# Performance work log

Measured on AMD Instinct MI355X. Metric: run time of the kernel, lower is better.

The kernel has to match this reference:

```python
import jax, jax.numpy as jnp
import numpy as np

HEADS = 16
DIM = 1024
D_K = DIM // HEADS
SEQ = 2048


def setup_inputs() -> dict:
    key = jax.random.key(0)
    ks = jax.random.split(key, 11)
    s = 1.0 / np.sqrt(DIM).astype(np.float32)
    return {
        "q": jax.random.normal(ks[0], (SEQ, DIM), jnp.float32),
        "k": jax.random.normal(ks[1], (SEQ, DIM), jnp.float32),
        "v": jax.random.normal(ks[2], (SEQ, DIM), jnp.float32),
        "Wq": jax.random.normal(ks[3], (DIM, DIM), jnp.float32) * s,
        "bq": jax.random.normal(ks[4], (DIM,), jnp.float32) * 0.01,
        "Wk": jax.random.normal(ks[5], (DIM, DIM), jnp.float32) * s,
        "bk": jax.random.normal(ks[6], (DIM,), jnp.float32) * 0.01,
        "Wv": jax.random.normal(ks[7], (DIM, DIM), jnp.float32) * s,
        "bv": jax.random.normal(ks[8], (DIM,), jnp.float32) * 0.01,
        "Wo": jax.random.normal(ks[9], (DIM, DIM), jnp.float32) * s,
        "bo": jax.random.normal(ks[10], (DIM,), jnp.float32) * 0.01,
    }


def reference(q, k, v, Wq, bq, Wk, bk, Wv, bv, Wo, bo):
    S = q.shape[0]
    # torch Linear: x @ W.T + b; view to (1, S, H, d_k) then transpose to (1, H, S, d_k)
    def proj(x, W, b):
        return (x @ W.T + b).reshape(1, S, HEADS, D_K).transpose(0, 2, 1, 3)

    qh = proj(q, Wq, bq)  # (1, H, S, d)
    kh = proj(k, Wk, bk)
    vh = proj(v, Wv, bv)

    scale = 1.0 / np.sqrt(D_K).astype(np.float32)
    scores = jnp.einsum("bhqd,bhkd->bhqk", qh, kh) * scale  # (1, H, S, S)
    # NOTE: source applies softmax over dim=1 == the HEADS axis (faithful quirk)
    attn = jax.nn.softmax(scores, axis=1)
    ctx = jnp.einsum("bhqk,bhkd->bhqd", attn, vh)  # (1, H, S, d)
    concat = ctx.transpose(0, 2, 1, 3).reshape(1, S, DIM)
    return concat @ Wo.T + bo
```

## Files before the change

### kernel.cpp

```cpp
#include <hip/hip_runtime.h>
#include <hip/hip_fp16.h>


typedef _Float16 f16;
typedef _Float16 f16x4 __attribute__((ext_vector_type(4)));
typedef _Float16 f16x8 __attribute__((ext_vector_type(8)));
typedef float    f32x4 __attribute__((ext_vector_type(4)));

#define S_LEN 2048
#define DIM   1024
#define NH    16
#define DK    64
#define SCALE 0.125f

#define MFMA(a, b, c) __builtin_amdgcn_mfma_f32_16x16x32_f16(a, b, c, 0, 0, 0)

typedef __attribute__((address_space(1))) void g_void;
typedef __attribute__((address_space(3))) void l_void;

static __device__ __forceinline__ void gload_lds16(const void* g, void* l) {
  __builtin_amdgcn_global_load_lds((g_void*)g, (l_void*)l, 16, 0, 0);
}

__global__ __launch_bounds__(256) void cvt_all(
    const float* __restrict__ q, const float* __restrict__ k, const float* __restrict__ v,
    const float* __restrict__ Wq, const float* __restrict__ Wk, const float* __restrict__ Wv,
    const float* __restrict__ Wo, f16* __restrict__ qh, f16* __restrict__ kh,
    f16* __restrict__ vh, f16* __restrict__ wqh, f16* __restrict__ wkh,
    f16* __restrict__ wvh, f16* __restrict__ woh) {
  const size_t M = 1048576;
  const int seg = blockIdx.y;
  const float* src;
  f16* dst;
  switch (seg) {
    case 0: src = q;      dst = qh;      break;
    case 1: src = q + M;  dst = qh + M;  break;
    case 2: src = k;      dst = kh;      break;
    case 3: src = k + M;  dst = kh + M;  break;
    case 4: src = v;      dst = vh;      break;
    case 5: src = v + M;  dst = vh + M;  break;
    case 6: src = Wq;     dst = wqh;     break;
    case 7: src = Wk;     dst = wkh;     break;
    case 8: src = Wv;     dst = wvh;     break;
    default: src = Wo;    dst = woh;     break;
  }
  int i = blockIdx.x * 256 + threadIdx.x;
  float4 vv = ((const float4*)src)[i];
  f16x4 o = {(f16)vv.x, (f16)vv.y, (f16)vv.z, (f16)vv.w};
  ((f16x4*)dst)[i] = o;
}

__global__ __launch_bounds__(256) void cvt_f32_f16(const float* __restrict__ src,
                                                   f16* __restrict__ dst, int n4) {
  int i = blockIdx.x * 256 + threadIdx.x;
  if (i < n4) {
    float4 v = ((const float4*)src)[i];
    f16x4 o = {(f16)v.x, (f16)v.y, (f16)v.z, (f16)v.w};
    ((f16x4*)dst)[i] = o;
  }
}

static __device__ __forceinline__ void gemm64_core(const f16* __restrict__ X,
                                                   const f16* __restrict__ W,
                                                   int k0, int k1, int bm, int bn,
                                                   f16* As2, f16* Bs2,
                                                   f32x4 (&acc)[4][2]) {
  const int tid = threadIdx.x;
  const int wv = tid >> 6;
  const int lane = tid & 63;
  const int qd = lane >> 4;
  const int l16 = lane & 15;
  const int wm = (wv & 1) * 64;
  const int wn = (wv >> 1) * 32;
  const int lr4 = lane >> 2, lc4 = lane & 3;
  const int kkw = wv & 1;
  const int rgw = wv >> 1;

  const f16* gA = X + (size_t)(bm + rgw * 64 + lr4) * DIM + k0 + kkw * 32 + lc4 * 8;
  const f16* gB = W + (size_t)(bn + rgw * 32 + lr4) * DIM + k0 + kkw * 32 + lc4 * 8;
  f16* lA = As2 + kkw * (128 * 32) + (rgw * 64) * 32;
  f16* lB = Bs2 + kkw * (64 * 32) + (rgw * 32) * 32;

  for (int kt = k0; kt < k1; kt += 64) {
#pragma unroll
    for (int t = 0; t < 4; t++)
      gload_lds16(gA + t * 16 * DIM, lA + t * 16 * 32);
#pragma unroll
    for (int t = 0; t < 2; t++)
      gload_lds16(gB + t * 16 * DIM, lB + t * 16 * 32);
    gA += 64;
    gB += 64;
    __syncthreads();

    f16x8 af[4][2], bf[2][2];
#pragma unroll
    for (int mi = 0; mi < 4; mi++)
#pragma unroll
      for (int kk = 0; kk < 2; kk++)
        af[mi][kk] = *(const f16x8*)&As2[kk * (128 * 32) + (wm + mi * 16 + l16) * 32 + qd * 8];
#pragma unroll
    for (int ni = 0; ni < 2; ni++)
#pragma unroll
      for (int kk = 0; kk < 2; kk++)
        bf[ni][kk] = *(const f16x8*)&Bs2[kk * (64 * 32) + (wn + ni * 16 + l16) * 32 + qd * 8];
#pragma unroll
    for (int mi = 0; mi < 4; mi++)
#pragma unroll
      for (int ni = 0; ni < 2; ni++) {
        acc[mi][ni] = MFMA(af[mi][0], bf[ni][0], acc[mi][ni]);
        acc[mi][ni] = MFMA(af[mi][1], bf[ni][1], acc[mi][ni]);
      }
    __syncthreads();
  }
}

__global__ __launch_bounds__(256) void gemm_qkv(
    const f16* __restrict__ X0, const f16* __restrict__ X1, const f16* __restrict__ X2,
    const f16* __restrict__ W0, const f16* __restrict__ W1, const f16* __restrict__ W2,
    const float* __restrict__ b0, const float* __restrict__ b1, const float* __restrict__ b2,
    f16* __restrict__ o0, f16* __restrict__ o1, f16* __restrict__ o2) {
  __shared__ __align__(16) f16 As2[2 * 128 * 32];
  __shared__ __align__(16) f16 Bs2[2 * 64 * 32];
  const int z = blockIdx.z;
  const f16* X = z == 0 ? X0 : z == 1 ? X1 : X2;
  const f16* W = z == 0 ? W0 : z == 1 ? W1 : W2;
  const float* bias = z == 0 ? b0 : z == 1 ? b1 : b2;
  f16* outh = z == 0 ? o0 : z == 1 ? o1 : o2;

  const int bm = blockIdx.y * 128, bn = blockIdx.x * 64;
  f32x4 acc[4][2];
#pragma unroll
  for (int a = 0; a < 4; a++)
#pragma unroll
    for (int b = 0; b < 2; b++) acc[a][b] = (f32x4){0.f, 0.f, 0.f, 0.f};

  gemm64_core(X, W, 0, DIM, bm, bn, As2, Bs2, acc);

  const int tid = threadIdx.x;
  const int wv = tid >> 6, lane = tid & 63;
  const int qd = lane >> 4, l16 = lane & 15;
  const int wm = (wv & 1) * 64, wn = (wv >> 1) * 32;
#pragma unroll
  for (int mi = 0; mi < 4; mi++) {
#pragma unroll
    for (int ni = 0; ni < 2; ni++) {
      const int gm = bm + wm + mi * 16 + qd * 4;
      const int gn = bn + wn + ni * 16 + l16;
      const float bs = bias[gn];
      if (z == 2) {
        f16x4 o = {(f16)(acc[mi][ni][0] + bs), (f16)(acc[mi][ni][1] + bs),
                   (f16)(acc[mi][ni][2] + bs), (f16)(acc[mi][ni][3] + bs)};
        *(f16x4*)&outh[(size_t)gn * S_LEN + gm] = o;
      } else {
#pragma unroll
        for (int r = 0; r < 4; r++)
          outh[(size_t)(gm + r) * DIM + gn] = (f16)(acc[mi][ni][r] + bs);
      }
    }
  }
}

__global__ __launch_bounds__(256) void gemm_out(const f16* __restrict__ X,
                                                const f16* __restrict__ W,
                                                const float* __restrict__ bias,
                                                float* __restrict__ outf) {
  __shared__ __align__(16) f16 As2[2 * 128 * 32];
  __shared__ __align__(16) f16 Bs2[2 * 64 * 32];
  const int z = blockIdx.z;
  const int bm = blockIdx.y * 128, bn = blockIdx.x * 64;
  f32x4 acc[4][2];
#pragma unroll
  for (int a = 0; a < 4; a++)
#pragma unroll
    for (int b = 0; b < 2; b++) acc[a][b] = (f32x4){0.f, 0.f, 0.f, 0.f};

  gemm64_core(X, W, z * (DIM / 2), (z + 1) * (DIM / 2), bm, bn, As2, Bs2, acc);

  const int tid = threadIdx.x;
  const int wv = tid >> 6, lane = tid & 63;
  const int qd = lane >> 4, l16 = lane & 15;
  const int wm = (wv & 1) * 64, wn = (wv >> 1) * 32;
#pragma unroll
  for (int mi = 0; mi < 4; mi++) {
#pragma unroll
    for (int ni = 0; ni < 2; ni++) {
      const int gm = bm + wm + mi * 16 + qd * 4;
      const int gn = bn + wn + ni * 16 + l16;
      const float bs = z == 0 ? bias[gn] : 0.f;
#pragma unroll
      for (int r = 0; r < 4; r++)
        atomicAdd(&outf[(size_t)(gm + r) * DIM + gn], acc[mi][ni][r] + bs);
    }
  }
}

__global__ __launch_bounds__(256) void attn_denom(const f16* __restrict__ Qp,
                                                  const f16* __restrict__ Kp,
                                                  f16* __restrict__ IDn) {
  __shared__ __align__(16) f16 Qs[2][2][64 * 32];
  __shared__ __align__(16) f16 Ks[2][2][64 * 32];
  const int tid = threadIdx.x;
  const int wv = tid >> 6;
  const int lane = tid & 63;
  const int qd = lane >> 4;
  const int l16 = lane & 15;
  const int wm = (wv & 1) * 32, wn = (wv >> 1) * 32;
  const int bi = blockIdx.y * 64, bj = blockIdx.x * 64;
  const int lr4 = lane >> 2, lc4 = lane & 3;
  const int hhw = wv & 1;
  const int kkw = wv >> 1;

  f32x4 dsum[2][2];
#pragma unroll
  for (int a = 0; a < 2; a++)
#pragma unroll
    for (int b = 0; b < 2; b++) dsum[a][b] = (f32x4){0.f, 0.f, 0.f, 0.f};

  for (int h0 = 0; h0 < NH; h0 += 2) {
    const int hcol = (h0 + hhw) * DK + kkw * 32;
    const f16* gq = Qp + (size_t)(bi + lr4) * DIM + hcol + lc4 * 8;
    const f16* gk = Kp + (size_t)(bj + lr4) * DIM + hcol + lc4 * 8;
#pragma unroll
    for (int t = 0; t < 4; t++) {
      gload_lds16(gq + (size_t)t * 16 * DIM, &Qs[hhw][kkw][t * 16 * 32]);
      gload_lds16(gk + (size_t)t * 16 * DIM, &Ks[hhw][kkw][t * 16 * 32]);
    }
    __syncthreads();

#pragma unroll
    for (int hh = 0; hh < 2; hh++) {
      f16x8 af[2][2], bf[2][2];
#pragma unroll
      for (int mi = 0; mi < 2; mi++)
#pragma unroll
        for (int kk = 0; kk < 2; kk++)
          af[mi][kk] = *(const f16x8*)&Qs[hh][kk][(wm + mi * 16 + l16) * 32 + qd * 8];
#pragma unroll
      for (int ni = 0; ni < 2; ni++)
#pragma unroll
        for (int kk = 0; kk < 2; kk++)
          bf[ni][kk] = *(const f16x8*)&Ks[hh][kk][(wn + ni * 16 + l16) * 32 + qd * 8];
#pragma unroll
      for (int mi = 0; mi < 2; mi++)
#pragma unroll
        for (int ni = 0; ni < 2; ni++) {
          f32x4 s = {0.f, 0.f, 0.f, 0.f};
          s = MFMA(af[mi][0], bf[ni][0], s);
          s = MFMA(af[mi][1], bf[ni][1], s);
#pragma unroll
          for (int r = 0; r < 4; r++) dsum[mi][ni][r] += __expf(s[r] * SCALE);
        }
    }
    __syncthreads();
  }
#pragma unroll
  for (int mi = 0; mi < 2; mi++)
#pragma unroll
    for (int ni = 0; ni < 2; ni++)
#pragma unroll
      for (int r = 0; r < 4; r++) {
        const int gi = bi + wm + mi * 16 + qd * 4 + r;
        const int gj = bj + wn + ni * 16 + l16;
        IDn[(size_t)gi * S_LEN + gj] = (f16)(1.f / dsum[mi][ni][r]);
      }
}

__global__ __launch_bounds__(256) void attn_ctx(const f16* __restrict__ Qp,
                                                const f16* __restrict__ Kp,
                                                const f16* __restrict__ Vt,
                                                const f16* __restrict__ IDn,
                                                float* __restrict__ Cp) {
  __shared__ __align__(16) f16 Ks[2][64 * 32];
  __shared__ __align__(16) f16 Vs[2][64 * 32];
  __shared__ __align__(16) f16 Is[2][128 * 32];
  __shared__ __align__(16) f16 Pl[4][32 * 32];
  const int tid = threadIdx.x;
  const int wv = tid >> 6;
  const int lane = tid & 63;
  const int qd = lane >> 4;
  const int l16 = lane & 15;
  const int h = blockIdx.y;
  const int i0 = blockIdx.x * 128;
  const int iw = i0 + wv * 32;
  const int jb = blockIdx.z * 512;
  const int lr4 = lane >> 2, lc4 = lane & 3;
  const int sw = wv & 1;
  const int gw = wv >> 1;
  f16* pl = Pl[wv];

  f16x8 aq[2][2];
#pragma unroll
  for (int mi = 0; mi < 2; mi++)
#pragma unroll
    for (int kk = 0; kk < 2; kk++)
      aq[mi][kk] = *(const f16x8*)(Qp + (size_t)(iw + mi * 16 + l16) * DIM +
                                   h * DK + kk * 32 + qd * 8);

  f32x4 acc[2][4];
#pragma unroll
  for (int a = 0; a < 2; a++)
#pragma unroll
    for (int b = 0; b < 4; b++) acc[a][b] = (f32x4){0.f, 0.f, 0.f, 0.f};

  for (int jt = 0; jt < 8; jt++) {
    const int j0 = jb + jt * 64;
#pragma unroll
    for (int t = 0; t < 2; t++)
      gload_lds16(Kp + (size_t)(j0 + gw * 32 + t * 16 + lr4) * DIM + h * DK + sw * 32 + lc4 * 8,
                  &Ks[sw][(gw * 32 + t * 16) * 32]);
#pragma unroll
    for (int t = 0; t < 2; t++)
      gload_lds16(Vt + (size_t)(h * DK + gw * 32 + t * 16 + lr4) * S_LEN + j0 + sw * 32 + lc4 * 8,
                  &Vs[sw][(gw * 32 + t * 16) * 32]);
#pragma unroll
    for (int t = 0; t < 4; t++)
      gload_lds16(IDn + (size_t)(i0 + gw * 64 + t * 16 + lr4) * S_LEN + j0 + sw * 32 + lc4 * 8,
                  &Is[sw][(gw * 64 + t * 16) * 32]);
    __syncthreads();

#pragma unroll
    for (int sub = 0; sub < 2; sub++) {
      f16x8 bk[2][2];
#pragma unroll
      for (int ni = 0; ni < 2; ni++)
#pragma unroll
        for (int kk = 0; kk < 2; kk++)
          bk[ni][kk] = *(const f16x8*)&Ks[kk][(sub * 32 + ni * 16 + l16) * 32 + qd * 8];
#pragma unroll
      for (int mi = 0; mi < 2; mi++)
#pragma unroll
        for (int ni = 0; ni < 2; ni++) {
          f32x4 s = {0.f, 0.f, 0.f, 0.f};
          s = MFMA(aq[mi][0], bk[ni][0], s);
          s = MFMA(aq[mi][1], bk[ni][1], s);
#pragma unroll
          for (int r = 0; r < 4; r++)
            pl[(mi * 16 + qd * 4 + r) * 32 + ni * 16 + l16] = (f16)__expf(s[r] * SCALE);
        }

      f16x8 bv[4];
#pragma unroll
      for (int nd = 0; nd < 4; nd++)
        bv[nd] = *(const f16x8*)&Vs[sub][(nd * 16 + l16) * 32 + qd * 8];
#pragma unroll
      for (int mi = 0; mi < 2; mi++) {
        f16x8 ef = *(const f16x8*)&pl[(mi * 16 + l16) * 32 + qd * 8];
        f16x8 idn = *(const f16x8*)&Is[sub][(wv * 32 + mi * 16 + l16) * 32 + qd * 8];
        f16x8 p = ef * idn;
#pragma unroll
        for (int nd = 0; nd < 4; nd++)
          acc[mi][nd] = MFMA(p, bv[nd], acc[mi][nd]);
      }
    }
    __syncthreads();
  }

#pragma unroll
  for (int mi = 0; mi < 2; mi++)
#pragma unroll
    for (int nd = 0; nd < 4; nd++)
#pragma unroll
      for (int r = 0; r < 4; r++)
        atomicAdd(&Cp[(size_t)(iw + mi * 16 + qd * 4 + r) * DIM + h * DK + nd * 16 + l16],
                  acc[mi][nd][r]);
}

extern "C" void kernel_launch(void* const* d_in, const int* in_sizes, int n_in,
                              void* d_out, int out_size, void* d_ws, size_t ws_size,
                              hipStream_t stream) {
  const float* q  = (const float*)d_in[0];
  const float* k  = (const float*)d_in[1];
  const float* v  = (const float*)d_in[2];
  const float* Wq = (const float*)d_in[3];
  const float* bq = (const float*)d_in[4];
  const float* Wk = (const float*)d_in[5];
  const float* bk = (const float*)d_in[6];
  const float* Wv = (const float*)d_in[7];
  const float* bv = (const float*)d_in[8];
  const float* Wo = (const float*)d_in[9];
  const float* bo = (const float*)d_in[10];
  float* out = (float*)d_out;

  f16* w = (f16*)d_ws;
  f16* qh  = w;
  f16* kh  = qh + (size_t)S_LEN * DIM;
  f16* vh  = kh + (size_t)S_LEN * DIM;
  f16* wqh = vh + (size_t)S_LEN * DIM;
  f16* wkh = wqh + (size_t)DIM * DIM;
  f16* wvh = wkh + (size_t)DIM * DIM;
  f16* woh = wvh + (size_t)DIM * DIM;
  f16* Qp  = woh + (size_t)DIM * DIM;
  f16* Kp  = Qp + (size_t)S_LEN * DIM;
  f16* Vt  = Kp + (size_t)S_LEN * DIM;
  f16* IDn = qh;
  float* Cp = (float*)vh;
  f16* Ct  = qh;

  dim3 b256(256);
  cvt_all<<<dim3(1024, 10), b256, 0, stream>>>(q, k, v, Wq, Wk, Wv, Wo,
                                               qh, kh, vh, wqh, wkh, wvh, woh);

  gemm_qkv<<<dim3(DIM / 64, S_LEN / 128, 3), b256, 0, stream>>>(
      qh, kh, vh, wqh, wkh, wvh, bq, bk, bv, Qp, Kp, Vt);

  hipMemsetAsync(Cp, 0, (size_t)S_LEN * DIM * sizeof(float), stream);
  hipMemsetAsync(out, 0, (size_t)S_LEN * DIM * sizeof(float), stream);

  attn_denom<<<dim3(S_LEN / 64, S_LEN / 64), b256, 0, stream>>>(Qp, Kp, IDn);
  attn_ctx<<<dim3(S_LEN / 128, NH, 4), b256, 0, stream>>>(Qp, Kp, Vt, IDn, Cp);

  const int nqkv4 = S_LEN * DIM / 4;
  cvt_f32_f16<<<nqkv4 / 256, b256, 0, stream>>>(Cp, Ct, nqkv4);

  gemm_out<<<dim3(DIM / 64, S_LEN / 128, 2), b256, 0, stream>>>(Ct, woh, bo, out);
}
```

Measured before the change: 233.3 us.

## Double-buffer LDS loads in attention kernels and load inverse denominators directly

Result: slower. 258.4 us (+10.8%).

```diff
diff --git a/kernel.cpp b/kernel.cpp
--- a/kernel.cpp
+++ b/kernel.cpp
@@ -14,6 +14,9 @@
 #define SCALE 0.125f
 
 #define MFMA(a, b, c) __builtin_amdgcn_mfma_f32_16x16x32_f16(a, b, c, 0, 0, 0)
+
+#define VM_WAIT0   asm volatile("s_waitcnt vmcnt(0)" ::: "memory")
+#define WG_BARRIER asm volatile("s_barrier" ::: "memory")
 
 typedef __attribute__((address_space(1))) void g_void;
 typedef __attribute__((address_space(3))) void l_void;
@@ -207,8 +210,8 @@
   const int wm = (wv & 1) * 32, wn = (wv >> 1) * 32;
   const int bi = blockIdx.y * 64, bj = blockIdx.x * 64;
   const int lr4 = lane >> 2, lc4 = lane & 3;
-  const int hhw = wv & 1;
-  const int kkw = wv >> 1;
+  const int kkw = wv & 1;
+  const int q0 = (wv >> 1) * 2;
 
   f32x4 dsum[2][2];
 #pragma unroll
@@ -216,42 +219,53 @@
 #pragma unroll
     for (int b = 0; b < 2; b++) dsum[a][b] = (f32x4){0.f, 0.f, 0.f, 0.f};
 
-  for (int h0 = 0; h0 < NH; h0 += 2) {
-    const int hcol = (h0 + hhw) * DK + kkw * 32;
-    const f16* gq = Qp + (size_t)(bi + lr4) * DIM + hcol + lc4 * 8;
-    const f16* gk = Kp + (size_t)(bj + lr4) * DIM + hcol + lc4 * 8;
-#pragma unroll
-    for (int t = 0; t < 4; t++) {
-      gload_lds16(gq + (size_t)t * 16 * DIM, &Qs[hhw][kkw][t * 16 * 32]);
-      gload_lds16(gk + (size_t)t * 16 * DIM, &Ks[hhw][kkw][t * 16 * 32]);
-    }
-    __syncthreads();
-
-#pragma unroll
-    for (int hh = 0; hh < 2; hh++) {
-      f16x8 af[2][2], bf[2][2];
-#pragma unroll
-      for (int mi = 0; mi < 2; mi++)
-#pragma unroll
-        for (int kk = 0; kk < 2; kk++)
-          af[mi][kk] = *(const f16x8*)&Qs[hh][kk][(wm + mi * 16 + l16) * 32 + qd * 8];
-#pragma unroll
-      for (int ni = 0; ni < 2; ni++)
-#pragma unroll
-        for (int kk = 0; kk < 2; kk++)
-          bf[ni][kk] = *(const f16x8*)&Ks[hh][kk][(wn + ni * 16 + l16) * 32 + qd * 8];
-#pragma unroll
-      for (int mi = 0; mi < 2; mi++)
-#pragma unroll
-        for (int ni = 0; ni < 2; ni++) {
-          f32x4 s = {0.f, 0.f, 0.f, 0.f};
-          s = MFMA(af[mi][0], bf[ni][0], s);
-          s = MFMA(af[mi][1], bf[ni][1], s);
-#pragma unroll
-          for (int r = 0; r < 4; r++) dsum[mi][ni][r] += __expf(s[r] * SCALE);
-        }
-    }
-    __syncthreads();
+  {
+    const f16* gq = Qp + (size_t)(bi + q0 * 16 + lr4) * DIM + 0 * DK + kkw * 32 + lc4 * 8;
+    const f16* gk = Kp + (size_t)(bj + q0 * 16 + lr4) * DIM + 0 * DK + kkw * 32 + lc4 * 8;
+#pragma unroll
+    for (int t = 0; t < 2; t++) {
+      gload_lds16(gq + (size_t)t * 16 * DIM, &Qs[0][kkw][(q0 + t) * 16 * 32]);
+      gload_lds16(gk + (size_t)t * 16 * DIM, &Ks[0][kkw][(q0 + t) * 16 * 32]);
+    }
+  }
+
+#pragma unroll
+  for (int h = 0; h < NH; h++) {
+    const int buf = h & 1;
+    VM_WAIT0;
+    WG_BARRIER;
+
+    if (h + 1 < NH) {
+      const f16* gq = Qp + (size_t)(bi + q0 * 16 + lr4) * DIM + (h + 1) * DK + kkw * 32 + lc4 * 8;
+      const f16* gk = Kp + (size_t)(bj + q0 * 16 + lr4) * DIM + (h + 1) * DK + kkw * 32 + lc4 * 8;
+#pragma unroll
+      for (int t = 0; t < 2; t++) {
+        gload_lds16(gq + (size_t)t * 16 * DIM, &Qs[buf ^ 1][kkw][(q0 + t) * 16 * 32]);
+        gload_lds16(gk + (size_t)t * 16 * DIM, &Ks[buf ^ 1][kkw][(q0 + t) * 16 * 32]);
+      }
+    }
+
+    f16x8 af[2][2], bf[2][2];
+#pragma unroll
+    for (int mi = 0; mi < 2; mi++)
+#pragma unroll
+      for (int kk = 0; kk < 2; kk++)
+        af[mi][kk] = *(const f16x8*)&Qs[buf][kk][(wm + mi * 16 + l16) * 32 + qd * 8];
+#pragma unroll
+    for (int ni = 0; ni < 2; ni++)
+#pragma unroll
+      for (int kk = 0; kk < 2; kk++)
+        bf[ni][kk] = *(const f16x8*)&Ks[buf][kk][(wn + ni * 16 + l16) * 32 + qd * 8];
+#pragma unroll
+    for (int mi = 0; mi < 2; mi++)
+#pragma unroll
+      for (int ni = 0; ni < 2; ni++) {
+        f32x4 s = {0.f, 0.f, 0.f, 0.f};
+        s = MFMA(af[mi][0], bf[ni][0], s);
+        s = MFMA(af[mi][1], bf[ni][1], s);
+#pragma unroll
+        for (int r = 0; r < 4; r++) dsum[mi][ni][r] += __expf(s[r] * SCALE);
+      }
   }
 #pragma unroll
   for (int mi = 0; mi < 2; mi++)
@@ -265,15 +279,14 @@
       }
 }
 
-__global__ __launch_bounds__(256) void attn_ctx(const f16* __restrict__ Qp,
-                                                const f16* __restrict__ Kp,
-                                                const f16* __restrict__ Vt,
-                                                const f16* __restrict__ IDn,
-                                                float* __restrict__ Cp) {
-  __shared__ __align__(16) f16 Ks[2][64 * 32];
+__global__ __launch_bounds__(256, 4) void attn_ctx(const f16* __restrict__ Qp,
+                                                   const f16* __restrict__ Kp,
+                                                   const f16* __restrict__ Vt,
+                                                   const f16* __restrict__ IDn,
+                                                   float* __restrict__ Cp) {
+  __shared__ __align__(16) f16 Ks[2][2][32 * 32];
   __shared__ __align__(16) f16 Vs[2][64 * 32];
-  __shared__ __align__(16) f16 Is[2][128 * 32];
-  __shared__ __align__(16) f16 Pl[4][32 * 32];
+  __shared__ __align__(16) f16 Pl[4][32 * 40];
   const int tid = threadIdx.x;
   const int wv = tid >> 6;
   const int lane = tid & 63;
@@ -284,8 +297,8 @@
   const int iw = i0 + wv * 32;
   const int jb = blockIdx.z * 512;
   const int lr4 = lane >> 2, lc4 = lane & 3;
-  const int sw = wv & 1;
-  const int gw = wv >> 1;
+  const int kkw = wv & 1;
+  const int rhw = wv >> 1;
   f16* pl = Pl[wv];
 
   f16x8 aq[2][2];
@@ -302,57 +315,67 @@
 #pragma unroll
     for (int b = 0; b < 4; b++) acc[a][b] = (f32x4){0.f, 0.f, 0.f, 0.f};
 
-  for (int jt = 0; jt < 8; jt++) {
-    const int j0 = jb + jt * 64;
-#pragma unroll
-    for (int t = 0; t < 2; t++)
-      gload_lds16(Kp + (size_t)(j0 + gw * 32 + t * 16 + lr4) * DIM + h * DK + sw * 32 + lc4 * 8,
-                  &Ks[sw][(gw * 32 + t * 16) * 32]);
-#pragma unroll
-    for (int t = 0; t < 2; t++)
-      gload_lds16(Vt + (size_t)(h * DK + gw * 32 + t * 16 + lr4) * S_LEN + j0 + sw * 32 + lc4 * 8,
-                  &Vs[sw][(gw * 32 + t * 16) * 32]);
-#pragma unroll
-    for (int t = 0; t < 4; t++)
-      gload_lds16(IDn + (size_t)(i0 + gw * 64 + t * 16 + lr4) * S_LEN + j0 + sw * 32 + lc4 * 8,
-                  &Is[sw][(gw * 64 + t * 16) * 32]);
-    __syncthreads();
-
-#pragma unroll
-    for (int sub = 0; sub < 2; sub++) {
-      f16x8 bk[2][2];
-#pragma unroll
-      for (int ni = 0; ni < 2; ni++)
-#pragma unroll
-        for (int kk = 0; kk < 2; kk++)
-          bk[ni][kk] = *(const f16x8*)&Ks[kk][(sub * 32 + ni * 16 + l16) * 32 + qd * 8];
+  f16x8 idn[2][2];
+
+  {
+    const int j0 = jb;
+    gload_lds16(Kp + (size_t)(j0 + rhw * 16 + lr4) * DIM + h * DK + kkw * 32 + lc4 * 8,
+                &Ks[0][kkw][(rhw * 16) * 32]);
+    gload_lds16(Vt + (size_t)(h * DK + wv * 16 + lr4) * S_LEN + j0 + lc4 * 8,
+                &Vs[0][(wv * 16) * 32]);
+#pragma unroll
+    for (int mi = 0; mi < 2; mi++)
+      idn[0][mi] = *(const f16x8*)(IDn + (size_t)(iw + mi * 16 + l16) * S_LEN + j0 + qd * 8);
+  }
+
+#pragma unroll
+  for (int jt = 0; jt < 16; jt++) {
+    const int buf = jt & 1;
+    VM_WAIT0;
+    WG_BARRIER;
+
+    if (jt + 1 < 16) {
+      const int j1 = jb + (jt + 1) * 32;
+      gload_lds16(Kp + (size_t)(j1 + rhw * 16 + lr4) * DIM + h * DK + kkw * 32 + lc4 * 8,
+                  &Ks[buf ^ 1][kkw][(rhw * 16) * 32]);
+      gload_lds16(Vt + (size_t)(h * DK + wv * 16 + lr4) * S_LEN + j1 + lc4 * 8,
+                  &Vs[buf ^ 1][(wv * 16) * 32]);
 #pragma unroll
       for (int mi = 0; mi < 2; mi++)
-#pragma unroll
-        for (int ni = 0; ni < 2; ni++) {
-          f32x4 s = {0.f, 0.f, 0.f, 0.f};
-          s = MFMA(aq[mi][0], bk[ni][0], s);
-          s = MFMA(aq[mi][1], bk[ni][1], s);
-#pragma unroll
-          for (int r = 0; r < 4; r++)
-            pl[(mi * 16 + qd * 4 + r) * 32 + ni * 16 + l16] = (f16)__expf(s[r] * SCALE);
-        }
-
-      f16x8 bv[4];
+        idn[buf ^ 1][mi] =
+            *(const f16x8*)(IDn + (size_t)(iw + mi * 16 + l16) * S_LEN + j1 + qd * 8);
+    }
+
+    f16x8 bk[2][2];
+#pragma unroll
+    for (int ni = 0; ni < 2; ni++)
+#pragma unroll
+      for (int kk = 0; kk < 2; kk++)
+        bk[ni][kk] = *(const f16x8*)&Ks[buf][kk][(ni * 16 + l16) * 32 + qd * 8];
+#pragma unroll
+    for (int mi = 0; mi < 2; mi++)
+#pragma unroll
+      for (int ni = 0; ni < 2; ni++) {
+        f32x4 s = {0.f, 0.f, 0.f, 0.f};
+        s = MFMA(aq[mi][0], bk[ni][0], s);
+        s = MFMA(aq[mi][1], bk[ni][1], s);
+#pragma unroll
+        for (int r = 0; r < 4; r++)
+          pl[(mi * 16 + qd * 4 + r) * 40 + ni * 16 + l16] = (f16)__expf(s[r] * SCALE);
+      }
+
+    f16x8 bv[4];
+#pragma unroll
+    for (int nd = 0; nd < 4; nd++)
+      bv[nd] = *(const f16x8*)&Vs[buf][(nd * 16 + l16) * 32 + qd * 8];
+#pragma unroll
+    for (int mi = 0; mi < 2; mi++) {
+      f16x8 ef = *(const f16x8*)&pl[(mi * 16 + l16) * 40 + qd * 8];
+      f16x8 p = ef * idn[buf][mi];
 #pragma unroll
       for (int nd = 0; nd < 4; nd++)
-        bv[nd] = *(const f16x8*)&Vs[sub][(nd * 16 + l16) * 32 + qd * 8];
-#pragma unroll
-      for (int mi = 0; mi < 2; mi++) {
-        f16x8 ef = *(const f16x8*)&pl[(mi * 16 + l16) * 32 + qd * 8];
-        f16x8 idn = *(const f16x8*)&Is[sub][(wv * 32 + mi * 16 + l16) * 32 + qd * 8];
-        f16x8 p = ef * idn;
-#pragma unroll
-        for (int nd = 0; nd < 4; nd++)
-          acc[mi][nd] = MFMA(p, bv[nd], acc[mi][nd]);
-      }
-    }
-    __syncthreads();
+        acc[mi][nd] = MFMA(p, bv[nd], acc[mi][nd]);
+    }
   }
 
 #pragma unroll
```
